# Kernel optimization log

Measured on AMD Instinct MI355X. Metric: run time of the kernel, lower is better.

## Reference

```python
import jax, jax.numpy as jnp
import numpy as np

N_NODES = 20000
N_EDGES = 160000
D_IN = 512
D_HID = 512
D_OUT = 512
N_GRAPHS = 128


def setup_inputs() -> dict:
    key = jax.random.key(0)
    ks = jax.random.split(key, 10)
    x = jax.random.normal(ks[0], (N_NODES, D_IN), dtype=jnp.float32)
    edge_index = jax.random.randint(ks[1], (2, N_EDGES), 0, N_NODES, dtype=jnp.int64)
    batch = jnp.sort(jax.random.randint(ks[2], (N_NODES,), 0, N_GRAPHS, dtype=jnp.int64))
    s = 1.0 / np.sqrt(D_IN)
    W1 = jax.random.normal(ks[3], (D_IN, D_HID), dtype=jnp.float32) * s
    b1 = jnp.zeros((D_HID,), dtype=jnp.float32)
    W2 = jax.random.normal(ks[4], (D_HID, D_OUT), dtype=jnp.float32) * s
    b2 = jnp.zeros((D_OUT,), dtype=jnp.float32)
    Wlin = jax.random.normal(ks[5], (D_OUT, D_OUT), dtype=jnp.float32) * s
    blin = jnp.zeros((D_OUT,), dtype=jnp.float32)
    return {"x": x, "edge_index": edge_index, "batch": batch,
            "W1": W1, "b1": b1, "W2": W2, "b2": b2, "Wlin": Wlin, "blin": blin}


def _gcn_conv(h, src, dst, W, b, n_nodes):
    # PyG GCNConv: h' = D^{-1/2} (A + I) D^{-1/2} (h @ W) + b, self-loops added.
    h = h @ W
    deg = jax.ops.segment_sum(jnp.ones_like(dst, dtype=h.dtype), dst, num_segments=n_nodes)
    dis = jnp.where(deg > 0, jax.lax.rsqrt(jnp.maximum(deg, 1.0)), 0.0)
    norm = dis[src] * dis[dst]                      # [E+N]
    msg = h[src] * norm[:, None]                    # gather-scale
    out = jax.ops.segment_sum(msg, dst, num_segments=n_nodes)  # scatter-add
    return out + b


def reference(x, edge_index, batch, W1, b1, W2, b2, Wlin, blin):
    n = x.shape[0]
    # StandardScaler: per-feature zero-mean, unit (population) std
    mu = jnp.mean(x, axis=0)
    sd = jnp.std(x, axis=0)
    xs = (x - mu) / jnp.where(sd > 0, sd, 1.0)
    # add self-loops once, shared by both convs
    ar = jnp.arange(n, dtype=edge_index.dtype)
    src = jnp.concatenate([edge_index[0], ar])
    dst = jnp.concatenate([edge_index[1], ar])
    x1 = jax.nn.relu(_gcn_conv(xs, src, dst, W1, b1, n))
    # dropout is identity in eval mode
    x2 = _gcn_conv(x1, src, dst, W2, b2, n)
    # global_mean_pool over graph ids
    sums = jax.ops.segment_sum(x2, batch, num_segments=N_GRAPHS)
    cnts = jax.ops.segment_sum(jnp.ones((n,), dtype=x2.dtype), batch, num_segments=N_GRAPHS)
    pooled = sums / jnp.maximum(cnts, 1.0)[:, None]
    # (second dropout also identity in eval); module returns x3 (pre log_softmax)
    return pooled @ Wlin + blin
```

## Files before the change

### kernel.cpp

```cpp
#include <hip/hip_runtime.h>
#include <hip/hip_bf16.h>


#define NN 20000
#define NE 160000
#define DD 512
#define NG 128
#define PKC 160
#define PNC 125

typedef __attribute__((ext_vector_type(8))) short bf16x8;
typedef __attribute__((ext_vector_type(4))) float f32x4;

static __device__ __forceinline__ short f2bf(float f) {
    union { float f; unsigned u; } a; a.f = f;
    unsigned r = a.u + 0x7FFF + ((a.u >> 16) & 1);
    return (short)(r >> 16);
}
static __device__ __forceinline__ float bf2f(short s) {
    union { unsigned u; float f; } a; a.u = ((unsigned)(unsigned short)s) << 16;
    return a.f;
}

__global__ __launch_bounds__(256) void colstats_kernel(const float* __restrict__ x,
                                                       float* __restrict__ colsum,
                                                       float* __restrict__ colsq) {
    int c = blockIdx.x * 256 + threadIdx.x;
    int r0 = blockIdx.y * 100;
    float s = 0.f, sq = 0.f;
    for (int r = r0; r < r0 + 100; ++r) {
        float v = x[(size_t)r * DD + c];
        s += v;
        sq = fmaf(v, v, sq);
    }
    atomicAdd(&colsum[c], s);
    atomicAdd(&colsq[c], sq);
}

__global__ void finalize_kernel(const float* __restrict__ colsum, const float* __restrict__ colsq,
                                float* __restrict__ rstd, float* __restrict__ murs) {
    int c = threadIdx.x;
    float m = colsum[c] * (1.0f / NN);
    float var = colsq[c] * (1.0f / NN) - m * m;
    float sd = sqrtf(fmaxf(var, 0.0f));
    float rs = (sd > 0.0f) ? (1.0f / sd) : 1.0f;
    rstd[c] = rs;
    murs[c] = m * rs;
}

__global__ __launch_bounds__(256) void xsplit_kernel(const float* __restrict__ x,
                                                     const float* __restrict__ rstd,
                                                     const float* __restrict__ murs,
                                                     short* __restrict__ xh,
                                                     short* __restrict__ xl) {
    int idx = blockIdx.x * 256 + threadIdx.x;
    int c4 = (idx & 127) * 4;
    float4 v = *(const float4*)(x + (size_t)idx * 4);
    float4 rs = *(const float4*)(rstd + c4);
    float4 ms = *(const float4*)(murs + c4);
    float s0 = fmaf(v.x, rs.x, -ms.x), s1 = fmaf(v.y, rs.y, -ms.y);
    float s2 = fmaf(v.z, rs.z, -ms.z), s3 = fmaf(v.w, rs.w, -ms.w);
    short h0 = f2bf(s0), h1 = f2bf(s1), h2 = f2bf(s2), h3 = f2bf(s3);
    *(short4*)(xh + (size_t)idx * 4) = make_short4(h0, h1, h2, h3);
    *(short4*)(xl + (size_t)idx * 4) =
        make_short4(f2bf(s0 - bf2f(h0)), f2bf(s1 - bf2f(h1)),
                    f2bf(s2 - bf2f(h2)), f2bf(s3 - bf2f(h3)));
}

__global__ __launch_bounds__(256) void wsplit_kernel(const float* __restrict__ W1,
                                                     short* __restrict__ Wh,
                                                     short* __restrict__ Wl) {
    __shared__ float t[32][33];
    int bk = blockIdx.x * 32, bn = blockIdx.y * 32;
    int r = threadIdx.x >> 5, c = threadIdx.x & 31;
#pragma unroll
    for (int i = 0; i < 4; ++i) {
        int rr = r + i * 8;
        t[rr][c] = W1[(size_t)(bk + rr) * DD + bn + c];
    }
    __syncthreads();
#pragma unroll
    for (int i = 0; i < 4; ++i) {
        int rr = r + i * 8;
        float v = t[c][rr];
        short h = f2bf(v);
        short l = f2bf(v - bf2f(h));
        Wh[(size_t)(bn + rr) * DD + bk + c] = h;
        Wl[(size_t)(bn + rr) * DD + bk + c] = l;
    }
}

__global__ void deginit_kernel(int* __restrict__ deg) {
    int i = blockIdx.x * 256 + threadIdx.x;
    if (i < NN) deg[i] = 1;
}

__global__ void degcount_kernel(const int* __restrict__ dst, int* __restrict__ deg, int es) {
    int e = blockIdx.x * 256 + threadIdx.x;
    if (e < NE) {
        int d = dst[(size_t)e * es];
        if ((unsigned)d < (unsigned)NN) atomicAdd(&deg[d], 1);
    }
}

__global__ void dis_kernel(const int* __restrict__ deg, float* __restrict__ dis) {
    int i = blockIdx.x * 256 + threadIdx.x;
    if (i < NN) dis[i] = rsqrtf((float)deg[i]);
}

__global__ __launch_bounds__(1024) void scan_kernel(const int* __restrict__ deg,
                                                    int* __restrict__ rowptr,
                                                    int* __restrict__ cursor) {
    const int PER = 20;
    __shared__ int sums[1024];
    int t = threadIdx.x;
    int base = t * PER;
    int local[PER];
    int s = 0;
#pragma unroll
    for (int j = 0; j < PER; ++j) {
        int idx = base + j;
        int v = (idx < NN) ? (deg[idx] - 1) : 0;
        local[j] = s;
        s += v;
    }
    sums[t] = s;
    __syncthreads();
    for (int off = 1; off < 1024; off <<= 1) {
        int v = (t >= off) ? sums[t - off] : 0;
        __syncthreads();
        sums[t] += v;
        __syncthreads();
    }
    int prefix = (t == 0) ? 0 : sums[t - 1];
#pragma unroll
    for (int j = 0; j < PER; ++j) {
        int idx = base + j;
        if (idx <= NN) {
            int val = prefix + local[j];
            rowptr[idx] = val;
            if (idx < NN) cursor[idx] = val;
        }
    }
}

__global__ void scatter_kernel(const int* __restrict__ src, const int* __restrict__ dst,
                               int* __restrict__ cursor, int* __restrict__ csrsrc, int es) {
    int e = blockIdx.x * 256 + threadIdx.x;
    if (e < NE) {
        int d = dst[(size_t)e * es];
        int sN = src[(size_t)e * es];
        if ((unsigned)d < (unsigned)NN && (unsigned)sN < (unsigned)NN) {
            int slot = atomicAdd(&cursor[d], 1);
            csrsrc[slot] = sN;
        }
    }
}

__global__ void cnode_kernel(const int* __restrict__ batch, int bs,
                             const float* __restrict__ dis, float* __restrict__ Cf) {
    int j = blockIdx.x * 256 + threadIdx.x;
    if (j < NN) {
        int G = batch[(size_t)j * bs];
        if ((unsigned)G < (unsigned)NG) {
            float d = dis[j];
            atomicAdd(&Cf[(size_t)G * NN + j], d * d);
        }
    }
}

__global__ void cedge_kernel(const int* __restrict__ src, const int* __restrict__ dst, int es,
                             const int* __restrict__ batch, int bs,
                             const float* __restrict__ dis, float* __restrict__ Cf) {
    int e = blockIdx.x * 256 + threadIdx.x;
    if (e < NE) {
        int i = dst[(size_t)e * es];
        int s = src[(size_t)e * es];
        if ((unsigned)i < (unsigned)NN && (unsigned)s < (unsigned)NN) {
            int G = batch[(size_t)i * bs];
            if ((unsigned)G < (unsigned)NG)
                atomicAdd(&Cf[(size_t)G * NN + s], dis[i] * dis[s]);
        }
    }
}

__global__ void invn_kernel(const int* __restrict__ batch, int bs, float* __restrict__ inv_n) {
    int g = threadIdx.x;
    int lo = 0, hi = NN;
    while (lo < hi) { int m = (lo + hi) >> 1; if (batch[(size_t)m * bs] < g) lo = m + 1; else hi = m; }
    int l0 = lo;
    lo = l0; hi = NN;
    while (lo < hi) { int m = (lo + hi) >> 1; if (batch[(size_t)m * bs] < g + 1) lo = m + 1; else hi = m; }
    inv_n[g] = 1.0f / fmaxf((float)(lo - l0), 1.0f);
}

__global__ __launch_bounds__(256) void gemm_mfma_kernel(const short* __restrict__ Ah_g,
                                                        const short* __restrict__ Al_g,
                                                        const short* __restrict__ Bh_g,
                                                        const short* __restrict__ Bl_g,
                                                        float* __restrict__ C,
                                                        int M) {
    __shared__ __attribute__((aligned(16))) short sAh[128][40];
    __shared__ __attribute__((aligned(16))) short sAl[128][40];
    __shared__ __attribute__((aligned(16))) short sBh[128][40];
    __shared__ __attribute__((aligned(16))) short sBl[128][40];
    int tid = threadIdx.x;
    int wave = tid >> 6, lane = tid & 63;
    int wm = (wave >> 1) * 64, wn = (wave & 1) * 64;
    int rowBase = blockIdx.x * 128, colBase = blockIdx.y * 128;
    int fr = lane & 15, kq = (lane >> 4) * 8;

    int s0 = tid, s1 = tid + 256;
    int r0 = s0 >> 2, k80 = (s0 & 3) * 8;
    int r1 = s1 >> 2, k81 = (s1 & 3) * 8;
    int ga0 = rowBase + r0, ga1 = rowBase + r1;
    int gb0 = colBase + r0, gb1 = colBase + r1;
    const bool av0 = ga0 < M, av1 = ga1 < M;

    f32x4 acc[4][4];
#pragma unroll
    for (int i = 0; i < 4; ++i)
#pragma unroll
        for (int j = 0; j < 4; ++j) acc[i][j] = (f32x4){0.f, 0.f, 0.f, 0.f};

    const bf16x8 z8 = {0, 0, 0, 0, 0, 0, 0, 0};
    bf16x8 rAh0, rAh1, rAl0, rAl1, rBh0, rBh1, rBl0, rBl1;

#define GLOAD(KK)                                                                      \
    do {                                                                               \
        rAh0 = av0 ? *(const bf16x8*)(Ah_g + (size_t)ga0 * DD + (KK) + k80) : z8;      \
        rAl0 = av0 ? *(const bf16x8*)(Al_g + (size_t)ga0 * DD + (KK) + k80) : z8;      \
        rAh1 = av1 ? *(const bf16x8*)(Ah_g + (size_t)ga1 * DD + (KK) + k81) : z8;      \
        rAl1 = av1 ? *(const bf16x8*)(Al_g + (size_t)ga1 * DD + (KK) + k81) : z8;      \
        rBh0 = *(const bf16x8*)(Bh_g + (size_t)gb0 * DD + (KK) + k80);                 \
        rBl0 = *(const bf16x8*)(Bl_g + (size_t)gb0 * DD + (KK) + k80);                 \
        rBh1 = *(const bf16x8*)(Bh_g + (size_t)gb1 * DD + (KK) + k81);                 \
        rBl1 = *(const bf16x8*)(Bl_g + (size_t)gb1 * DD + (KK) + k81);                 \
    } while (0)

    GLOAD(0);
    for (int step = 0; step < 16; ++step) {
        *(bf16x8*)&sAh[r0][k80] = rAh0;  *(bf16x8*)&sAl[r0][k80] = rAl0;
        *(bf16x8*)&sAh[r1][k81] = rAh1;  *(bf16x8*)&sAl[r1][k81] = rAl1;
        *(bf16x8*)&sBh[r0][k80] = rBh0;  *(bf16x8*)&sBl[r0][k80] = rBl0;
        *(bf16x8*)&sBh[r1][k81] = rBh1;  *(bf16x8*)&sBl[r1][k81] = rBl1;
        __syncthreads();
        if (step < 15) GLOAD((step + 1) * 32);

        bf16x8 fah[4], fal[4], fbh[4], fbl[4];
#pragma unroll
        for (int mi = 0; mi < 4; ++mi) {
            fah[mi] = *(const bf16x8*)&sAh[wm + mi * 16 + fr][kq];
            fal[mi] = *(const bf16x8*)&sAl[wm + mi * 16 + fr][kq];
        }
#pragma unroll
        for (int ni = 0; ni < 4; ++ni) {
            fbh[ni] = *(const bf16x8*)&sBh[wn + ni * 16 + fr][kq];
            fbl[ni] = *(const bf16x8*)&sBl[wn + ni * 16 + fr][kq];
        }
#pragma unroll
        for (int mi = 0; mi < 4; ++mi)
#pragma unroll
            for (int ni = 0; ni < 4; ++ni) {
                acc[mi][ni] = __builtin_amdgcn_mfma_f32_16x16x32_bf16(fah[mi], fbh[ni], acc[mi][ni], 0, 0, 0);
                acc[mi][ni] = __builtin_amdgcn_mfma_f32_16x16x32_bf16(fah[mi], fbl[ni], acc[mi][ni], 0, 0, 0);
                acc[mi][ni] = __builtin_amdgcn_mfma_f32_16x16x32_bf16(fal[mi], fbh[ni], acc[mi][ni], 0, 0, 0);
            }
        __syncthreads();
    }
#undef GLOAD

#pragma unroll
    for (int mi = 0; mi < 4; ++mi)
#pragma unroll
        for (int ni = 0; ni < 4; ++ni) {
            int col = colBase + wn + ni * 16 + fr;
            int row0 = rowBase + wm + mi * 16 + (lane >> 4) * 4;
#pragma unroll
            for (int r = 0; r < 4; ++r) {
                int row = row0 + r;
                if (row < M) C[(size_t)row * DD + col] = acc[mi][ni][r];
            }
        }
}

__global__ __launch_bounds__(256) void agg_kernel(const float* __restrict__ h,
                                                  float* __restrict__ out,
                                                  const float* __restrict__ dis,
                                                  const int* __restrict__ rowptr,
                                                  const int* __restrict__ csrsrc,
                                                  const float* __restrict__ bias,
                                                  int relu) {
    int i = blockIdx.x;
    int f = threadIdx.x * 2;
    float di = dis[i];
    float2 v = *(const float2*)(h + (size_t)i * DD + f);
    float accx = di * v.x, accy = di * v.y;
    int e0 = rowptr[i], e1 = rowptr[i + 1];
    if (e0 < e1) {
        int s = csrsrc[e0];
        float ds = dis[s];
        for (int e = e0; e < e1; ++e) {
            int   sn = 0;
            float dn = 0.f;
            if (e + 1 < e1) { sn = csrsrc[e + 1]; dn = dis[sn]; }
            float2 hv = *(const float2*)(h + (size_t)s * DD + f);
            accx = fmaf(ds, hv.x, accx);
            accy = fmaf(ds, hv.y, accy);
            s = sn; ds = dn;
        }
    }
    accx = fmaf(di, accx, bias[f]);
    accy = fmaf(di, accy, bias[f + 1]);
    if (relu) { accx = fmaxf(accx, 0.f); accy = fmaxf(accy, 0.f); }
    *(float2*)(out + (size_t)i * DD + f) = make_float2(accx, accy);
}

__global__ __launch_bounds__(256) void pgemm_kernel(const float* __restrict__ A,
                                                    const float* __restrict__ B,
                                                    float* __restrict__ part) {
    __shared__ float As[16][132];
    __shared__ float Bs[16][128];
    int tid = threadIdx.x;
    int tx = tid & 15, ty = tid >> 4;
    int colBase = blockIdx.x * 128;
    int kc = blockIdx.y;
    int kBase = kc * PKC;

    float acc[8][8];
#pragma unroll
    for (int i = 0; i < 8; ++i)
#pragma unroll
        for (int j = 0; j < 8; ++j) acc[i][j] = 0.f;

    for (int k0 = kBase; k0 < kBase + PKC; k0 += 16) {
#pragma unroll
        for (int i = 0; i < 2; ++i) {
            int lin = tid + i * 256;
            int r = lin >> 2, c4 = (lin & 3) * 4;
            float4 v = *(const float4*)(A + (size_t)r * NN + k0 + c4);
            As[c4 + 0][r] = v.x;
            As[c4 + 1][r] = v.y;
            As[c4 + 2][r] = v.z;
            As[c4 + 3][r] = v.w;
        }
#pragma unroll
        for (int i = 0; i < 2; ++i) {
            int lin = tid + i * 256;
            int kk = lin >> 5, c4 = (lin & 31) * 4;
            *(float4*)&Bs[kk][c4] = *(const float4*)(B + (size_t)(k0 + kk) * DD + colBase + c4);
        }
        __syncthreads();
#pragma unroll
        for (int kk = 0; kk < 16; ++kk) {
            float a[8], b[8];
            *(float4*)&a[0] = *(const float4*)&As[kk][ty * 4];
            *(float4*)&a[4] = *(const float4*)&As[kk][64 + ty * 4];
            *(float4*)&b[0] = *(const float4*)&Bs[kk][tx * 4];
            *(float4*)&b[4] = *(const float4*)&Bs[kk][64 + tx * 4];
#pragma unroll
            for (int i = 0; i < 8; ++i)
#pragma unroll
                for (int j = 0; j < 8; ++j) acc[i][j] = fmaf(a[i], b[j], acc[i][j]);
        }
        __syncthreads();
    }

    float* dst = part + (size_t)kc * NG * DD;
#pragma unroll
    for (int i = 0; i < 8; ++i) {
        int r = (i < 4) ? (ty * 4 + i) : (64 + ty * 4 + (i - 4));
        int c0 = colBase + tx * 4;
        int c1c = colBase + 64 + tx * 4;
        *(float4*)(dst + (size_t)r * DD + c0) =
            make_float4(acc[i][0], acc[i][1], acc[i][2], acc[i][3]);
        *(float4*)(dst + (size_t)r * DD + c1c) =
            make_float4(acc[i][4], acc[i][5], acc[i][6], acc[i][7]);
    }
}

__global__ __launch_bounds__(64) void reduce_kernel(const float* __restrict__ part,
                                                    const float* __restrict__ inv_n,
                                                    float* __restrict__ pooled) {
    int e = blockIdx.x * 64 + threadIdx.x;
    float s = 0.f;
#pragma unroll 5
    for (int sl = 0; sl < PNC; ++sl)
        s += part[(size_t)sl * (NG * DD) + e];
    pooled[e] = s * inv_n[e >> 9];
}

__global__ __launch_bounds__(256) void tail_kernel(const float* __restrict__ src,
                                                   const float* __restrict__ W,
                                                   const float* __restrict__ bias,
                                                   float* __restrict__ dst) {
    __shared__ float p[DD];
    __shared__ float red[4][64];
    int g = blockIdx.x;
    int colBase = blockIdx.y * 64;
    int tid = threadIdx.x;
    int c = tid & 63, ks = tid >> 6;
    p[tid] = src[(size_t)g * DD + tid];
    p[tid + 256] = src[(size_t)g * DD + tid + 256];
    __syncthreads();
    int col = colBase + c;
    float acc = 0.f;
    int k0 = ks * 128;
#pragma unroll 8
    for (int k = k0; k < k0 + 128; ++k)
        acc = fmaf(p[k], W[(size_t)k * DD + col], acc);
    red[ks][c] = acc;
    __syncthreads();
    if (ks == 0)
        dst[(size_t)g * DD + col] = red[0][c] + red[1][c] + red[2][c] + red[3][c] + bias[col];
}

extern "C" void kernel_launch(void* const* d_in, const int* in_sizes, int n_in,
                              void* d_out, int out_size, void* d_ws, size_t ws_size,
                              hipStream_t stream) {
    const float* x    = (const float*)d_in[0];
    const int*   ei   = (const int*)d_in[1];
    const int*   batch= (const int*)d_in[2];
    const float* W1   = (const float*)d_in[3];
    const float* b1   = (const float*)d_in[4];
    const float* W2   = (const float*)d_in[5];
    const float* b2   = (const float*)d_in[6];
    const float* Wlin = (const float*)d_in[7];
    const float* blin = (const float*)d_in[8];
    float* out = (float*)d_out;

    const int es = (in_sizes[1] == 2 * 2 * NE) ? 2 : 1;
    const int bs = (in_sizes[2] == 2 * NN) ? 2 : 1;
    const int* esrc = ei;
    const int* edst = ei + (size_t)NE * es;

    char* w = (char*)d_ws;
    auto alloc = [&](size_t bytes) { void* p = (void*)w; w += (bytes + 255) & ~(size_t)255; return p; };
    float* h      = (float*)alloc((size_t)NN * DD * 4);
    float* part   = h;
    float* g      = (float*)alloc((size_t)NN * DD * 4);
    short* xh     = (short*)g;
    short* xl     = (short*)g + (size_t)NN * DD;
    short* W1h    = (short*)alloc((size_t)DD * DD * 2);
    short* W1l    = (short*)alloc((size_t)DD * DD * 2);
    float* Cf     = (float*)alloc((size_t)NG * NN * 4);
    float* pooled = (float*)alloc((size_t)NG * DD * 4);
    float* tbuf   = (float*)alloc((size_t)NG * DD * 4);
    float* inv_n  = (float*)alloc(NG * 4);
    float* rstd   = (float*)alloc(DD * 4);
    float* murs   = (float*)alloc(DD * 4);
    float* stats  = (float*)alloc(2 * DD * 4);
    float* dis    = (float*)alloc(NN * 4);
    int*   deg    = (int*)alloc(NN * 4);
    int*   rowptr = (int*)alloc((NN + 4) * 4);
    int*   cursor = (int*)alloc(NN * 4);
    int*   csrsrc = (int*)alloc(NE * 4);
    float* colsum = stats;
    float* colsq  = stats + DD;

    hipMemsetAsync(stats, 0, 2 * DD * 4, stream);
    colstats_kernel<<<dim3(2, 200), 256, 0, stream>>>(x, colsum, colsq);
    finalize_kernel<<<1, 512, 0, stream>>>(colsum, colsq, rstd, murs);
    xsplit_kernel<<<10000, 256, 0, stream>>>(x, rstd, murs, xh, xl);
    wsplit_kernel<<<dim3(16, 16), 256, 0, stream>>>(W1, W1h, W1l);

    deginit_kernel<<<(NN + 255) / 256, 256, 0, stream>>>(deg);
    degcount_kernel<<<NE / 256, 256, 0, stream>>>(edst, deg, es);
    dis_kernel<<<(NN + 255) / 256, 256, 0, stream>>>(deg, dis);
    scan_kernel<<<1, 1024, 0, stream>>>(deg, rowptr, cursor);
    scatter_kernel<<<NE / 256, 256, 0, stream>>>(esrc, edst, cursor, csrsrc, es);

    hipMemsetAsync(Cf, 0, (size_t)NG * NN * 4, stream);
    cnode_kernel<<<(NN + 255) / 256, 256, 0, stream>>>(batch, bs, dis, Cf);
    cedge_kernel<<<NE / 256, 256, 0, stream>>>(esrc, edst, es, batch, bs, dis, Cf);
    invn_kernel<<<1, NG, 0, stream>>>(batch, bs, inv_n);

    gemm_mfma_kernel<<<dim3((NN + 127) / 128, DD / 128), 256, 0, stream>>>(xh, xl, W1h, W1l, h, NN);
    agg_kernel<<<NN, 256, 0, stream>>>(h, g, dis, rowptr, csrsrc, b1, 1);
    pgemm_kernel<<<dim3(4, PNC), 256, 0, stream>>>(Cf, g, part);
    reduce_kernel<<<1024, 64, 0, stream>>>(part, inv_n, pooled);
    tail_kernel<<<dim3(NG, 8), 256, 0, stream>>>(pooled, W2, b2, tbuf);
    tail_kernel<<<dim3(NG, 8), 256, 0, stream>>>(tbuf, Wlin, blin, out);
}
```

Baseline: 352.2 us.

## Store GEMM output as bf16 and merge small graph-setup kernels

```diff
diff --git a/kernel.cpp b/kernel.cpp
--- a/kernel.cpp
+++ b/kernel.cpp
@@ -90,11 +90,6 @@
     }
 }
 
-__global__ void deginit_kernel(int* __restrict__ deg) {
-    int i = blockIdx.x * 256 + threadIdx.x;
-    if (i < NN) deg[i] = 1;
-}
-
 __global__ void degcount_kernel(const int* __restrict__ dst, int* __restrict__ deg, int es) {
     int e = blockIdx.x * 256 + threadIdx.x;
     if (e < NE) {
@@ -103,9 +98,24 @@
     }
 }
 
-__global__ void dis_kernel(const int* __restrict__ deg, float* __restrict__ dis) {
-    int i = blockIdx.x * 256 + threadIdx.x;
-    if (i < NN) dis[i] = rsqrtf((float)deg[i]);
+__global__ __launch_bounds__(256) void dis_invn_kernel(const int* __restrict__ deg,
+                                                       float* __restrict__ dis,
+                                                       const int* __restrict__ batch, int bs,
+                                                       float* __restrict__ inv_n) {
+    if (blockIdx.x < 79) {
+        int i = blockIdx.x * 256 + threadIdx.x;
+        if (i < NN) dis[i] = rsqrtf((float)(deg[i] + 1));
+    } else {
+        int g = threadIdx.x;
+        if (g < NG) {
+            int lo = 0, hi = NN;
+            while (lo < hi) { int m = (lo + hi) >> 1; if (batch[(size_t)m * bs] < g) lo = m + 1; else hi = m; }
+            int l0 = lo;
+            lo = l0; hi = NN;
+            while (lo < hi) { int m = (lo + hi) >> 1; if (batch[(size_t)m * bs] < g + 1) lo = m + 1; else hi = m; }
+            inv_n[g] = 1.0f / fmaxf((float)(lo - l0), 1.0f);
+        }
+    }
 }
 
 __global__ __launch_bounds__(1024) void scan_kernel(const int* __restrict__ deg,
@@ -120,7 +130,7 @@
 #pragma unroll
     for (int j = 0; j < PER; ++j) {
         int idx = base + j;
-        int v = (idx < NN) ? (deg[idx] - 1) : 0;
+        int v = (idx < NN) ? deg[idx] : 0;
         local[j] = s;
         s += v;
     }
@@ -157,23 +167,18 @@
     }
 }
 
-__global__ void cnode_kernel(const int* __restrict__ batch, int bs,
-                             const float* __restrict__ dis, float* __restrict__ Cf) {
-    int j = blockIdx.x * 256 + threadIdx.x;
-    if (j < NN) {
-        int G = batch[(size_t)j * bs];
+__global__ void cfbuild_kernel(const int* __restrict__ src, const int* __restrict__ dst, int es,
+                               const int* __restrict__ batch, int bs,
+                               const float* __restrict__ dis, float* __restrict__ Cf) {
+    int idx = blockIdx.x * 256 + threadIdx.x;
+    if (idx < NN) {
+        int G = batch[(size_t)idx * bs];
         if ((unsigned)G < (unsigned)NG) {
-            float d = dis[j];
-            atomicAdd(&Cf[(size_t)G * NN + j], d * d);
-        }
-    }
-}
-
-__global__ void cedge_kernel(const int* __restrict__ src, const int* __restrict__ dst, int es,
-                             const int* __restrict__ batch, int bs,
-                             const float* __restrict__ dis, float* __restrict__ Cf) {
-    int e = blockIdx.x * 256 + threadIdx.x;
-    if (e < NE) {
+            float d = dis[idx];
+            atomicAdd(&Cf[(size_t)G * NN + idx], d * d);
+        }
+    } else if (idx < NN + NE) {
+        int e = idx - NN;
         int i = dst[(size_t)e * es];
         int s = src[(size_t)e * es];
         if ((unsigned)i < (unsigned)NN && (unsigned)s < (unsigned)NN) {
@@ -184,21 +189,11 @@
     }
 }
 
-__global__ void invn_kernel(const int* __restrict__ batch, int bs, float* __restrict__ inv_n) {
-    int g = threadIdx.x;
-    int lo = 0, hi = NN;
-    while (lo < hi) { int m = (lo + hi) >> 1; if (batch[(size_t)m * bs] < g) lo = m + 1; else hi = m; }
-    int l0 = lo;
-    lo = l0; hi = NN;
-    while (lo < hi) { int m = (lo + hi) >> 1; if (batch[(size_t)m * bs] < g + 1) lo = m + 1; else hi = m; }
-    inv_n[g] = 1.0f / fmaxf((float)(lo - l0), 1.0f);
-}
-
 __global__ __launch_bounds__(256) void gemm_mfma_kernel(const short* __restrict__ Ah_g,
                                                         const short* __restrict__ Al_g,
                                                         const short* __restrict__ Bh_g,
                                                         const short* __restrict__ Bl_g,
-                                                        float* __restrict__ C,
+                                                        unsigned short* __restrict__ Ch,
                                                         int M) {
     __shared__ __attribute__((aligned(16))) short sAh[128][40];
     __shared__ __attribute__((aligned(16))) short sAl[128][40];
@@ -279,12 +274,12 @@
 #pragma unroll
             for (int r = 0; r < 4; ++r) {
                 int row = row0 + r;
-                if (row < M) C[(size_t)row * DD + col] = acc[mi][ni][r];
+                if (row < M) Ch[(size_t)row * DD + col] = (unsigned short)f2bf(acc[mi][ni][r]);
             }
         }
 }
 
-__global__ __launch_bounds__(256) void agg_kernel(const float* __restrict__ h,
+__global__ __launch_bounds__(256) void agg_kernel(const unsigned short* __restrict__ h,
                                                   float* __restrict__ out,
                                                   const float* __restrict__ dis,
                                                   const int* __restrict__ rowptr,
@@ -294,8 +289,8 @@
     int i = blockIdx.x;
     int f = threadIdx.x * 2;
     float di = dis[i];
-    float2 v = *(const float2*)(h + (size_t)i * DD + f);
-    float accx = di * v.x, accy = di * v.y;
+    ushort2 v = *(const ushort2*)(h + (size_t)i * DD + f);
+    float accx = di * bf2f((short)v.x), accy = di * bf2f((short)v.y);
     int e0 = rowptr[i], e1 = rowptr[i + 1];
     if (e0 < e1) {
         int s = csrsrc[e0];
@@ -304,9 +299,9 @@
             int   sn = 0;
             float dn = 0.f;
             if (e + 1 < e1) { sn = csrsrc[e + 1]; dn = dis[sn]; }
-            float2 hv = *(const float2*)(h + (size_t)s * DD + f);
-            accx = fmaf(ds, hv.x, accx);
-            accy = fmaf(ds, hv.y, accy);
+            ushort2 hv = *(const ushort2*)(h + (size_t)s * DD + f);
+            accx = fmaf(ds, bf2f((short)hv.x), accx);
+            accy = fmaf(ds, bf2f((short)hv.y), accy);
             s = sn; ds = dn;
         }
     }
@@ -436,47 +431,45 @@
 
     char* w = (char*)d_ws;
     auto alloc = [&](size_t bytes) { void* p = (void*)w; w += (bytes + 255) & ~(size_t)255; return p; };
-    float* h      = (float*)alloc((size_t)NN * DD * 4);
-    float* part   = h;
+    float* hreg   = (float*)alloc((size_t)NN * DD * 4);
+    unsigned short* hb = (unsigned short*)hreg;
+    float* part   = hreg;
     float* g      = (float*)alloc((size_t)NN * DD * 4);
     short* xh     = (short*)g;
     short* xl     = (short*)g + (size_t)NN * DD;
     short* W1h    = (short*)alloc((size_t)DD * DD * 2);
     short* W1l    = (short*)alloc((size_t)DD * DD * 2);
     float* Cf     = (float*)alloc((size_t)NG * NN * 4);
+    float* stats  = (float*)alloc(2 * DD * 4);
+    int*   deg    = (int*)alloc(NN * 4);
+    size_t zbytes = (size_t)((char*)deg + (size_t)NN * 4 - (char*)Cf);
     float* pooled = (float*)alloc((size_t)NG * DD * 4);
     float* tbuf   = (float*)alloc((size_t)NG * DD * 4);
     float* inv_n  = (float*)alloc(NG * 4);
     float* rstd   = (float*)alloc(DD * 4);
     float* murs   = (float*)alloc(DD * 4);
-    float* stats  = (float*)alloc(2 * DD * 4);
     float* dis    = (float*)alloc(NN * 4);
-    int*   deg    = (int*)alloc(NN * 4);
     int*   rowptr = (int*)alloc((NN + 4) * 4);
     int*   cursor = (int*)alloc(NN * 4);
     int*   csrsrc = (int*)alloc(NE * 4);
     float* colsum = stats;
     float* colsq  = stats + DD;
 
-    hipMemsetAsync(stats, 0, 2 * DD * 4, stream);
+    hipMemsetAsync(Cf, 0, zbytes, stream);
     colstats_kernel<<<dim3(2, 200), 256, 0, stream>>>(x, colsum, colsq);
     finalize_kernel<<<1, 512, 0, stream>>>(colsum, colsq, rstd, murs);
     xsplit_kernel<<<10000, 256, 0, stream>>>(x, rstd, murs, xh, xl);
     wsplit_kernel<<<dim3(16, 16), 256, 0, stream>>>(W1, W1h, W1l);
 
-    deginit_kernel<<<(NN + 255) / 256, 256, 0, stream>>>(deg);
     degcount_kernel<<<NE / 256, 256, 0, stream>>>(edst, deg, es);
-    dis_kernel<<<(NN + 255) / 256, 256, 0, stream>>>(deg, dis);
+    dis_invn_kernel<<<80, 256, 0, stream>>>(deg, dis, batch, bs, inv_n);
     scan_kernel<<<1, 1024, 0, stream>>>(deg, rowptr, cursor);
     scatter_kernel<<<NE / 256, 256, 0, stream>>>(esrc, edst, cursor, csrsrc, es);
 
-    hipMemsetAsync(Cf, 0, (size_t)NG * NN * 4, stream);
-    cnode_kernel<<<(NN + 255) / 256, 256, 0, stream>>>(batch, bs, dis, Cf);
-    cedge_kernel<<<NE / 256, 256, 0, stream>>>(esrc, edst, es, batch, bs, dis, Cf);
-    invn_kernel<<<1, NG, 0, stream>>>(batch, bs, inv_n);
-
-    gemm_mfma_kernel<<<dim3((NN + 127) / 128, DD / 128), 256, 0, stream>>>(xh, xl, W1h, W1l, h, NN);
-    agg_kernel<<<NN, 256, 0, stream>>>(h, g, dis, rowptr, csrsrc, b1, 1);
+    cfbuild_kernel<<<(NN + NE + 255) / 256, 256, 0, stream>>>(esrc, edst, es, batch, bs, dis, Cf);
+
+    gemm_mfma_kernel<<<dim3((NN + 127) / 128, DD / 128), 256, 0, stream>>>(xh, xl, W1h, W1l, hb, NN);
+    agg_kernel<<<NN, 256, 0, stream>>>(hb, g, dis, rowptr, csrsrc, b1, 1);
     pgemm_kernel<<<dim3(4, PNC), 256, 0, stream>>>(Cf, g, part);
     reduce_kernel<<<1024, 64, 0, stream>>>(part, inv_n, pooled);
     tail_kernel<<<dim3(NG, 8), 256, 0, stream>>>(pooled, W2, b2, tbuf);
```

New measurement: 339.5 us. -3.6%, faster.
